# Optimization experiments

Hardware: AMD Instinct MI355X
Metric: run time of the kernel (lower is better)

## Reference

```python
import jax, jax.numpy as jnp
import numpy as np

B, C, H, W = 256, 2048, 16, 8
NUM_CLASSES = 10000
SCALE = 1.0  # cls_layer.s for cls_type='Linear', scale=1
N_ITERS = 20


def setup_inputs() -> dict:
    key = jax.random.key(0)
    k1, k2, k3 = jax.random.split(key, 3)
    features = jax.random.normal(k1, (B, C, H, W), dtype=jnp.float32)
    targets = jax.random.randint(k2, (B,), 0, NUM_CLASSES)
    # nn.init.normal_(self.weight, std=0.01)
    weight = jax.random.normal(k3, (NUM_CLASSES, C), dtype=jnp.float32) * 0.01
    return {"features": features, "targets": targets, "weight": weight}


def reference(features, targets, weight):
    # 1) GlobalAvgPool over H,W then squeeze -> [B, C]; bottleneck is identity
    #    (embedding_dim=0, with_bnneck=False).
    neck_feat = features.mean(axis=(2, 3))
    t = neck_feat.shape[0]

    # cls_type == 'Linear': logits = F.linear(neck_feat, weight); cls_layer is
    # a pass-through, so every loop iteration computes identical quantities
    # (the random 'maskarea' in the original is overwritten before use).
    logits = jnp.einsum('bc,nc->bn', neck_feat, weight)  # [B, num_classes]
    soft = jax.nn.softmax(logits, axis=1)

    # right_prob = softmax probability at the target class (scatter+mul+sum)
    right_prob = jnp.take_along_axis(soft, targets[:, None], axis=1)[:, 0]  # [t]

    # All N_ITERS iterations append the same right_prob, so at the final
    # iteration: mean == right_prob, variance over iterations == 0.
    mean_sl = right_prob                      # [t]
    var_sl = jnp.zeros_like(right_prob)       # [t]
    con = mean_sl / (var_sl * 1e4)            # -> +inf (matches torch div-by-0)
    ri = jnp.tanh(1.2 * con)                  # tanh(inf) = 1.0
    # new_weight[i] = t * ri[i] / ri.sum()
    new_weight = (t * ri / ri.sum())[None, :]  # [1, t]

    cls_outputs = logits                       # Linear cls layer is identity
    pred_class_logits = logits * SCALE
    feat = neck_feat                           # neck_feat == 'before', bottleneck identity
    return cls_outputs, pred_class_logits, feat, new_weight
```

## Files before the change

kernel.cpp:

```cpp
#include <hip/hip_runtime.h>


#define OUT1_OFF (256 * 10000)
#define FEAT_OFF (2 * 256 * 10000)
#define NW_OFF   (2 * 256 * 10000 + 256 * 2048)

typedef __attribute__((ext_vector_type(4))) float f32x4;
typedef __attribute__((ext_vector_type(8))) short bf16x8;
typedef __attribute__((ext_vector_type(4))) unsigned int u32x4;

__device__ inline unsigned pk2bf(float lo, float hi) {
    unsigned a = __float_as_uint(lo), b = __float_as_uint(hi);
    unsigned ra = (a + 0x7FFFu + ((a >> 16) & 1u)) >> 16;
    unsigned rb = (b + 0x7FFFu + ((b >> 16) & 1u)) & 0xFFFF0000u;
    return ra | rb;
}

__global__ __launch_bounds__(256) void pool_kernel(
    const float* __restrict__ f, float* __restrict__ out,
    unsigned int* __restrict__ wsA32) {
    int tid = threadIdx.x;
    int g = tid >> 5;
    int l = tid & 31;
    int r0 = blockIdx.x * 16 + g * 2;
    const f32x4* s0 = (const f32x4*)(f + (size_t)r0 * 128);
    f32x4 v0 = s0[l];
    f32x4 v1 = s0[l + 32];
    float a = v0[0] + v0[1] + v0[2] + v0[3];
    float b = v1[0] + v1[1] + v1[2] + v1[3];
#pragma unroll
    for (int off = 16; off >= 1; off >>= 1) {
        a += __shfl_xor(a, off);
        b += __shfl_xor(b, off);
    }
    if (l == 0) {
        float m0 = a * (1.0f / 128.0f), m1 = b * (1.0f / 128.0f);
        float2 fv; fv.x = m0; fv.y = m1;
        *(float2*)&out[FEAT_OFF + r0] = fv;
        int bb = r0 >> 11, c = r0 & 2047;
        int chunk = ((bb >> 4) * 256 + (c >> 3)) * 16 + (bb & 15);
        wsA32[chunk * 4 + ((c & 7) >> 1)] = pk2bf(m0, m1);
    }
    if (blockIdx.x == 0) out[NW_OFF + tid] = 1.0f;
}

__global__ __launch_bounds__(512) void gemm_kernel(
    const u32x4* __restrict__ A16, const float* __restrict__ W,
    float* __restrict__ out) {
    int tid = threadIdx.x;
    int n0 = blockIdx.x * 64;
    int wid = tid >> 6, lane = tid & 63;
    int wm = wid >> 1, wn = wid & 1;
    int r = lane & 15, q = lane >> 4;

    const u32x4* paBase = A16 + q * 16 + r;
    int wmBase = wm * 16384;

    int row0 = n0 + wn * 32 + r;
    if (row0 > 9999) row0 = 9999;
    int row1 = row0 + 16;
    if (row1 > 9999) row1 = 9999;
    const f32x4* pB0 = (const f32x4*)(W + (size_t)row0 * 2048) + q * 2;
    const f32x4* pB1 = (const f32x4*)(W + (size_t)row1 * 2048) + q * 2;

    f32x4 acc[4][2];
#pragma unroll
    for (int i = 0; i < 4; ++i)
#pragma unroll
        for (int j = 0; j < 2; ++j) acc[i][j] = (f32x4){0.f, 0.f, 0.f, 0.f};

    u32x4 Xa0, Xa1, Xa2, Xa3, Xa4, Xa5, Xa6, Xa7;
    f32x4 Xb0, Xb1, Xb2, Xb3, Xb4, Xb5, Xb6, Xb7;
    u32x4 Ya0, Ya1, Ya2, Ya3, Ya4, Ya5, Ya6, Ya7;
    f32x4 Yb0, Yb1, Yb2, Yb3, Yb4, Yb5, Yb6, Yb7;

#define ISSUE(S, kt)                                      \
    {                                                     \
        const u32x4* pa = paBase + (kt) * 128;            \
        S##a0 = pa[wmBase];                               \
        S##a1 = pa[wmBase + 64];                          \
        S##a2 = pa[wmBase + 4096];                        \
        S##a3 = pa[wmBase + 4160];                        \
        S##a4 = pa[wmBase + 8192];                        \
        S##a5 = pa[wmBase + 8256];                        \
        S##a6 = pa[wmBase + 12288];                       \
        S##a7 = pa[wmBase + 12352];                       \
        S##b0 = pB0[(kt)*16];                             \
        S##b1 = pB0[(kt)*16 + 1];                         \
        S##b2 = pB0[(kt)*16 + 8];                         \
        S##b3 = pB0[(kt)*16 + 9];                         \
        S##b4 = pB1[(kt)*16];                             \
        S##b5 = pB1[(kt)*16 + 1];                         \
        S##b6 = pB1[(kt)*16 + 8];                         \
        S##b7 = pB1[(kt)*16 + 9];                         \
    }

#define CVT(bv, p0, p1)                  \
    {                                    \
        u32x4 t;                         \
        t.x = pk2bf(p0[0], p0[1]);       \
        t.y = pk2bf(p0[2], p0[3]);       \
        t.z = pk2bf(p1[0], p1[1]);       \
        t.w = pk2bf(p1[2], p1[3]);       \
        bv = *(bf16x8*)&t;               \
    }

#define MF(i, a_, bv, j)                                       \
    acc[i][j] = __builtin_amdgcn_mfma_f32_16x16x32_bf16(       \
        *(bf16x8*)&a_, bv, acc[i][j], 0, 0, 0)

#define COMPUTE(S)                                                          \
    {                                                                       \
        bf16x8 bv;                                                          \
        CVT(bv, S##b0, S##b1);                                \
        MF(0, S##a0, bv, 0); MF(1, S##a2, bv, 0);                           \
        MF(2, S##a4, bv, 0); MF(3, S##a6, bv, 0);                           \
        CVT(bv, S##b2, S##b3);                                \
        MF(0, S##a1, bv, 0); MF(1, S##a3, bv, 0);                           \
        MF(2, S##a5, bv, 0); MF(3, S##a7, bv, 0);                           \
        CVT(bv, S##b4, S##b5);                                \
        MF(0, S##a0, bv, 1); MF(1, S##a2, bv, 1);                           \
        MF(2, S##a4, bv, 1); MF(3, S##a6, bv, 1);                           \
        CVT(bv, S##b6, S##b7);                                \
        MF(0, S##a1, bv, 1); MF(1, S##a3, bv, 1);                           \
        MF(2, S##a5, bv, 1); MF(3, S##a7, bv, 1);                           \
    }

    ISSUE(X, 0);
    ISSUE(Y, 1);
    for (int kt = 0; kt < 30; kt += 2) {
        COMPUTE(X);
        ISSUE(X, kt + 2);
        COMPUTE(Y);
        ISSUE(Y, kt + 3);
    }
    COMPUTE(X);
    COMPUTE(Y);

#pragma unroll
    for (int i = 0; i < 4; ++i)
#pragma unroll
        for (int j = 0; j < 2; ++j) {
            int n = n0 + (wn * 2 + j) * 16 + r;
            if (n < 10000) {
                int mbase = (wm * 4 + i) * 16 + q * 4;
#pragma unroll
                for (int qq = 0; qq < 4; ++qq) {
                    float v = acc[i][j][qq];
                    size_t off = (size_t)(mbase + qq) * 10000 + n;
                    out[off] = v;
                    out[OUT1_OFF + off] = v;
                }
            }
        }
#undef ISSUE
#undef CVT
#undef MF
#undef COMPUTE
}

extern "C" void kernel_launch(void* const* d_in, const int* in_sizes, int n_in,
                              void* d_out, int out_size, void* d_ws, size_t ws_size,
                              hipStream_t stream) {
    const float* feats = (const float*)d_in[0];
    const float* weight = (const float*)d_in[2];
    float* out = (float*)d_out;

    pool_kernel<<<32768, 256, 0, stream>>>(feats, out, (unsigned int*)d_ws);
    gemm_kernel<<<157, 512, 0, stream>>>((const u32x4*)d_ws, weight, out);
}
```

Baseline: 128.2 us.

## Restructure GEMM to single-wave blocks covering all 256 rows per 16 classes

The GEMM now launches 625 single-wavefront blocks, each computing all 256 batch rows for 16 classes. Each weight row is read and converted to bf16 exactly once, where before each weight row was handled by several waves. The pool kernel writes the bf16 activations in a new layout so each lane loads 16 contiguous A fragments per k-step. In exchange, the whole 1 MB activation matrix is re-read by every block (relying on L2), each wave holds 64 accumulator registers, and only one wave per block is available to hide latency.

```diff
diff --git a/kernel.cpp b/kernel.cpp
--- a/kernel.cpp
+++ b/kernel.cpp
@@ -38,97 +38,72 @@
         float2 fv; fv.x = m0; fv.y = m1;
         *(float2*)&out[FEAT_OFF + r0] = fv;
         int bb = r0 >> 11, c = r0 & 2047;
-        int chunk = ((bb >> 4) * 256 + (c >> 3)) * 16 + (bb & 15);
-        wsA32[chunk * 4 + ((c & 7) >> 1)] = pk2bf(m0, m1);
+        int kt = c >> 5, q = (c >> 3) & 3, rr = bb & 15, mf = bb >> 4;
+        int chunk2 = (kt * 64 + q * 16 + rr) * 16 + mf;
+        wsA32[chunk2 * 4 + ((c & 7) >> 1)] = pk2bf(m0, m1);
     }
     if (blockIdx.x == 0) out[NW_OFF + tid] = 1.0f;
 }
 
-__global__ __launch_bounds__(512) void gemm_kernel(
+__global__ __launch_bounds__(64) void gemm_kernel(
     const u32x4* __restrict__ A16, const float* __restrict__ W,
     float* __restrict__ out) {
-    int tid = threadIdx.x;
-    int n0 = blockIdx.x * 64;
-    int wid = tid >> 6, lane = tid & 63;
-    int wm = wid >> 1, wn = wid & 1;
+    int lane = threadIdx.x;
     int r = lane & 15, q = lane >> 4;
+    int bn0 = blockIdx.x * 16;
 
-    const u32x4* paBase = A16 + q * 16 + r;
-    int wmBase = wm * 16384;
+    const u32x4* pa = A16 + lane * 16;
+    const f32x4* pw = (const f32x4*)(W + (size_t)(bn0 + r) * 2048) + q * 2;
 
-    int row0 = n0 + wn * 32 + r;
-    if (row0 > 9999) row0 = 9999;
-    int row1 = row0 + 16;
-    if (row1 > 9999) row1 = 9999;
-    const f32x4* pB0 = (const f32x4*)(W + (size_t)row0 * 2048) + q * 2;
-    const f32x4* pB1 = (const f32x4*)(W + (size_t)row1 * 2048) + q * 2;
+    f32x4 acc[16];
+#pragma unroll
+    for (int i = 0; i < 16; ++i) acc[i] = (f32x4){0.f, 0.f, 0.f, 0.f};
 
-    f32x4 acc[4][2];
-#pragma unroll
-    for (int i = 0; i < 4; ++i)
-#pragma unroll
-        for (int j = 0; j < 2; ++j) acc[i][j] = (f32x4){0.f, 0.f, 0.f, 0.f};
+    u32x4 Xa0, Xa1, Xa2, Xa3, Xa4, Xa5, Xa6, Xa7,
+          Xa8, Xa9, Xa10, Xa11, Xa12, Xa13, Xa14, Xa15;
+    u32x4 Ya0, Ya1, Ya2, Ya3, Ya4, Ya5, Ya6, Ya7,
+          Ya8, Ya9, Ya10, Ya11, Ya12, Ya13, Ya14, Ya15;
+    f32x4 Xw0, Xw1, Yw0, Yw1;
 
-    u32x4 Xa0, Xa1, Xa2, Xa3, Xa4, Xa5, Xa6, Xa7;
-    f32x4 Xb0, Xb1, Xb2, Xb3, Xb4, Xb5, Xb6, Xb7;
-    u32x4 Ya0, Ya1, Ya2, Ya3, Ya4, Ya5, Ya6, Ya7;
-    f32x4 Yb0, Yb1, Yb2, Yb3, Yb4, Yb5, Yb6, Yb7;
-
-#define ISSUE(S, kt)                                      \
-    {                                                     \
-        const u32x4* pa = paBase + (kt) * 128;            \
-        S##a0 = pa[wmBase];                               \
-        S##a1 = pa[wmBase + 64];                          \
-        S##a2 = pa[wmBase + 4096];                        \
-        S##a3 = pa[wmBase + 4160];                        \
-        S##a4 = pa[wmBase + 8192];                        \
-        S##a5 = pa[wmBase + 8256];                        \
-        S##a6 = pa[wmBase + 12288];                       \
-        S##a7 = pa[wmBase + 12352];                       \
-        S##b0 = pB0[(kt)*16];                             \
-        S##b1 = pB0[(kt)*16 + 1];                         \
-        S##b2 = pB0[(kt)*16 + 8];                         \
-        S##b3 = pB0[(kt)*16 + 9];                         \
-        S##b4 = pB1[(kt)*16];                             \
-        S##b5 = pB1[(kt)*16 + 1];                         \
-        S##b6 = pB1[(kt)*16 + 8];                         \
-        S##b7 = pB1[(kt)*16 + 9];                         \
+#define ISSUE(S, kt)                                    \
+    {                                                   \
+        const u32x4* p = pa + (kt) * 1024;              \
+        S##w0 = pw[(kt) * 8];                           \
+        S##w1 = pw[(kt) * 8 + 1];                       \
+        S##a0 = p[0];   S##a1 = p[1];                   \
+        S##a2 = p[2];   S##a3 = p[3];                   \
+        S##a4 = p[4];   S##a5 = p[5];                   \
+        S##a6 = p[6];   S##a7 = p[7];                   \
+        S##a8 = p[8];   S##a9 = p[9];                   \
+        S##a10 = p[10]; S##a11 = p[11];                 \
+        S##a12 = p[12]; S##a13 = p[13];                 \
+        S##a14 = p[14]; S##a15 = p[15];                 \
     }
 
-#define CVT(bv, p0, p1)                  \
-    {                                    \
-        u32x4 t;                         \
-        t.x = pk2bf(p0[0], p0[1]);       \
-        t.y = pk2bf(p0[2], p0[3]);       \
-        t.z = pk2bf(p1[0], p1[1]);       \
-        t.w = pk2bf(p1[2], p1[3]);       \
-        bv = *(bf16x8*)&t;               \
-    }
+#define MF(mf, a_, bv) \
+    acc[mf] = __builtin_amdgcn_mfma_f32_16x16x32_bf16(*(bf16x8*)&a_, bv, acc[mf], 0, 0, 0)
 
-#define MF(i, a_, bv, j)                                       \
-    acc[i][j] = __builtin_amdgcn_mfma_f32_16x16x32_bf16(       \
-        *(bf16x8*)&a_, bv, acc[i][j], 0, 0, 0)
-
-#define COMPUTE(S)                                                          \
-    {                                                                       \
-        bf16x8 bv;                                                          \
-        CVT(bv, S##b0, S##b1);                                \
-        MF(0, S##a0, bv, 0); MF(1, S##a2, bv, 0);                           \
-        MF(2, S##a4, bv, 0); MF(3, S##a6, bv, 0);                           \
-        CVT(bv, S##b2, S##b3);                                \
-        MF(0, S##a1, bv, 0); MF(1, S##a3, bv, 0);                           \
-        MF(2, S##a5, bv, 0); MF(3, S##a7, bv, 0);                           \
-        CVT(bv, S##b4, S##b5);                                \
-        MF(0, S##a0, bv, 1); MF(1, S##a2, bv, 1);                           \
-        MF(2, S##a4, bv, 1); MF(3, S##a6, bv, 1);                           \
-        CVT(bv, S##b6, S##b7);                                \
-        MF(0, S##a1, bv, 1); MF(1, S##a3, bv, 1);                           \
-        MF(2, S##a5, bv, 1); MF(3, S##a7, bv, 1);                           \
+#define COMPUTE(S)                                                 \
+    {                                                              \
+        u32x4 t;                                                   \
+        t.x = pk2bf(S##w0[0], S##w0[1]);                           \
+        t.y = pk2bf(S##w0[2], S##w0[3]);                           \
+        t.z = pk2bf(S##w1[0], S##w1[1]);                           \
+        t.w = pk2bf(S##w1[2], S##w1[3]);                           \
+        bf16x8 bv = *(bf16x8*)&t;                                  \
+        MF(0, S##a0, bv);   MF(1, S##a1, bv);                      \
+        MF(2, S##a2, bv);   MF(3, S##a3, bv);                      \
+        MF(4, S##a4, bv);   MF(5, S##a5, bv);                      \
+        MF(6, S##a6, bv);   MF(7, S##a7, bv);                      \
+        MF(8, S##a8, bv);   MF(9, S##a9, bv);                      \
+        MF(10, S##a10, bv); MF(11, S##a11, bv);                    \
+        MF(12, S##a12, bv); MF(13, S##a13, bv);                    \
+        MF(14, S##a14, bv); MF(15, S##a15, bv);                    \
     }
 
     ISSUE(X, 0);
     ISSUE(Y, 1);
-    for (int kt = 0; kt < 30; kt += 2) {
+    for (int kt = 0; kt < 62; kt += 2) {
         COMPUTE(X);
         ISSUE(X, kt + 2);
         COMPUTE(Y);
@@ -138,23 +113,16 @@
     COMPUTE(Y);
 
 #pragma unroll
-    for (int i = 0; i < 4; ++i)
+    for (int mf = 0; mf < 16; ++mf) {
 #pragma unroll
-        for (int j = 0; j < 2; ++j) {
-            int n = n0 + (wn * 2 + j) * 16 + r;
-            if (n < 10000) {
-                int mbase = (wm * 4 + i) * 16 + q * 4;
-#pragma unroll
-                for (int qq = 0; qq < 4; ++qq) {
-                    float v = acc[i][j][qq];
-                    size_t off = (size_t)(mbase + qq) * 10000 + n;
-                    out[off] = v;
-                    out[OUT1_OFF + off] = v;
-                }
-            }
+        for (int j = 0; j < 4; ++j) {
+            size_t off = (size_t)(mf * 16 + q * 4 + j) * 10000 + bn0 + r;
+            float v = acc[mf][j];
+            out[off] = v;
+            out[OUT1_OFF + off] = v;
         }
+    }
 #undef ISSUE
-#undef CVT
 #undef MF
 #undef COMPUTE
 }
@@ -167,5 +135,5 @@
     float* out = (float*)d_out;
 
     pool_kernel<<<32768, 256, 0, stream>>>(feats, out, (unsigned int*)d_ws);
-    gemm_kernel<<<157, 512, 0, stream>>>((const u32x4*)d_ws, weight, out);
+    gemm_kernel<<<625, 64, 0, stream>>>((const u32x4*)d_ws, weight, out);
 }
```

New measurement: 151.4 us. 1.18x slower.
